# Kernel tuning notes

Measured on AMD Instinct MI355X. Metric: run time of the kernel, lower is better.

## Reference

```python
import jax, jax.numpy as jnp
import numpy as np

DIM_Q = 512
DIM_K = 512
DIM_V = 512
NUM_HEADS = 8
B, NQ, NK = 4, 2048, 2048


def _linear_init(key, d_in, d_out):
    kw, kb = jax.random.split(key)
    bound = 1.0 / np.sqrt(d_in)
    W = jax.random.uniform(kw, (d_in, d_out), minval=-bound, maxval=bound, dtype=jnp.float32)
    b = jax.random.uniform(kb, (d_out,), minval=-bound, maxval=bound, dtype=jnp.float32)
    return W, b


def setup_inputs() -> dict:
    key = jax.random.key(0)
    ks = jax.random.split(key, 6)
    Q = jax.random.normal(ks[0], (B, NQ, DIM_Q), dtype=jnp.float32)
    K = jax.random.normal(ks[1], (B, NK, DIM_K), dtype=jnp.float32)
    Wq, bq = _linear_init(ks[2], DIM_Q, DIM_V)
    Wk, bk = _linear_init(ks[3], DIM_K, DIM_V)
    Wv, bv = _linear_init(ks[4], DIM_K, DIM_V)
    Wo, bo = _linear_init(ks[5], DIM_V, DIM_V)
    ln0_g = jnp.ones((DIM_V,), jnp.float32)
    ln0_b = jnp.zeros((DIM_V,), jnp.float32)
    ln1_g = jnp.ones((DIM_V,), jnp.float32)
    ln1_b = jnp.zeros((DIM_V,), jnp.float32)
    return {"Q": Q, "K": K, "Wq": Wq, "bq": bq, "Wk": Wk, "bk": bk,
            "Wv": Wv, "bv": bv, "Wo": Wo, "bo": bo,
            "ln0_g": ln0_g, "ln0_b": ln0_b, "ln1_g": ln1_g, "ln1_b": ln1_b}


def _layer_norm(x, g, b, eps=1e-5):
    mu = jnp.mean(x, axis=-1, keepdims=True)
    var = jnp.mean(jnp.square(x - mu), axis=-1, keepdims=True)
    return (x - mu) * jax.lax.rsqrt(var + eps) * g + b


def reference(Q, K, Wq, bq, Wk, bk, Wv, bv, Wo, bo, ln0_g, ln0_b, ln1_g, ln1_b):
    h = NUM_HEADS
    dh = DIM_V // h
    q = Q @ Wq + bq                      # [B, NQ, DIM_V]
    k = K @ Wk + bk                      # [B, NK, DIM_V]
    v = K @ Wv + bv                      # [B, NK, DIM_V]
    qh = q.reshape(B, NQ, h, dh)
    kh = k.reshape(B, NK, h, dh)
    vh = v.reshape(B, NK, h, dh)
    # NOTE: faithful to original — scale by sqrt(dim_V), not sqrt(head_dim)
    scores = jnp.einsum('bqhd,bkhd->bhqk', qh, kh) / jnp.sqrt(jnp.float32(DIM_V))
    A = jax.nn.softmax(scores, axis=-1)  # [B, h, NQ, NK]
    o = jnp.einsum('bhqk,bkhd->bqhd', A, vh) + qh
    H = o.reshape(B, NQ, DIM_V)          # residual with projected Q
    H = _layer_norm(H, ln0_g, ln0_b)
    H = H + jax.nn.relu(H @ Wo + bo)
    H = _layer_norm(H, ln1_g, ln1_b)
    return H
```

## Files before the change

kernel.cpp:

```cpp
#include <hip/hip_runtime.h>

typedef float f32x4 __attribute__((ext_vector_type(4)));
typedef float f32x16 __attribute__((ext_vector_type(16)));
typedef __bf16 bf16x8 __attribute__((ext_vector_type(8)));
typedef unsigned short u16;
typedef unsigned int u32;
typedef u16 u16x8 __attribute__((ext_vector_type(8)));
typedef u16 u16x4 __attribute__((ext_vector_type(4)));
typedef u32 u32x4 __attribute__((ext_vector_type(4)));

#define SCALE2F (0.044194173824159216f * 1.4426950408889634f)
#define UNSCALE (1.0f / SCALE2F)

__device__ __forceinline__ u16 f2bf(float x){ return __builtin_bit_cast(u16, (__bf16)x); }
__device__ __forceinline__ float bf2f(u16 h){ unsigned u = ((unsigned)h) << 16; return __builtin_bit_cast(float, u); }
__device__ __forceinline__ int swz(int r, int byteInRow){ return (r*128 + byteInRow) ^ ((r & 7) << 4); }
__device__ __forceinline__ void gload16(const void* g, void* l) {
  __builtin_amdgcn_global_load_lds(
      (const __attribute__((address_space(1))) void*)g,
      (__attribute__((address_space(3))) void*)l, 16, 0, 0);
}
__device__ __forceinline__ u32 cvtpk(float lo, float hi_) {
  u32 r;
  asm("v_cvt_pk_bf16_f32 %0, %1, %2" : "=v"(r) : "v"(lo), "v"(hi_));
  return r;
}
__device__ __forceinline__ void swap32(u32 &a, u32 &b) {
  asm("v_permlane32_swap_b32 %0, %1" : "+v"(a), "+v"(b));
}

#define MFMA(a,b,c)   __builtin_amdgcn_mfma_f32_16x16x32_bf16((a),(b),(c),0,0,0)
#define MFMA32(a,b,c) __builtin_amdgcn_mfma_f32_32x32x16_bf16((a),(b),(c),0,0,0)

__global__ __launch_bounds__(256) void wprep_k(
    const float* __restrict__ W0, const float* __restrict__ W1,
    const float* __restrict__ W2, const float* __restrict__ W3,
    u16* __restrict__ wt)
{
  __shared__ float tile[64][68];
  const float* Ws[4] = {W0, W1, W2, W3};
  const float* W = Ws[blockIdx.z];
  const float sc = (blockIdx.z == 0) ? SCALE2F : 1.0f;
  u16* out = wt + (size_t)blockIdx.z * 512 * 512;
  int k0 = blockIdx.x * 64, n0 = blockIdx.y * 64;
  int t = threadIdx.x;
  #pragma unroll
  for (int i = 0; i < 2; ++i) {
    int c = t + i*256; int r = c >> 3, k8 = c & 7;
    const float* src = W + (size_t)(k0 + r)*512 + n0 + k8*8;
    *(f32x4*)&tile[r][k8*8]     = *(const f32x4*)src;
    *(f32x4*)&tile[r][k8*8 + 4] = *(const f32x4*)(src + 4);
  }
  __syncthreads();
  #pragma unroll
  for (int i = 0; i < 2; ++i) {
    int c = t + i*256; int r = c >> 3, k8 = c & 7;
    u16x8 h;
    #pragma unroll
    for (int j = 0; j < 8; ++j) h[j] = f2bf(tile[k8*8 + j][r] * sc);
    *(u16x8*)(out + (size_t)(n0 + r)*512 + k0 + k8*8) = h;
  }
}

__global__ __launch_bounds__(512) void proj2_k(
    const float* __restrict__ Qin, const float* __restrict__ Kin,
    const u16* __restrict__ wt,
    const float* __restrict__ bq, const float* __restrict__ bk, const float* __restrict__ bv,
    u16* __restrict__ qbuf, u16* __restrict__ kbuf, u16* __restrict__ vt)
{
  __shared__ __align__(16) u16 lA[2][64*64];
  __shared__ __align__(16) u16 lB0[2][128*64];
  __shared__ __align__(16) u16 lB1[2][128*64];
  int z = blockIdx.z;
  const float* A     = z ? Kin : Qin;
  const u16*   Bt0   = wt + (size_t)(z ? 1 : 0) * 262144;
  const u16*   Bt1   = wt + (size_t)2 * 262144;
  const float* bias0 = z ? bk : bq;
  const float bscale = z ? 1.0f : SCALE2F;
  int row0 = blockIdx.x * 64, col0 = blockIdx.y * 128;
  int t = threadIdx.x, lane = t & 63, wid = t >> 6;
  int wr = wid >> 2, wc = wid & 3;
  int l15 = lane & 15, lg = lane >> 4;
  int ar = t >> 3, ak8 = t & 7;
  int br = t >> 3;
  int bsrc = (((t & 7) << 4) ^ ((br & 7) << 4)) >> 1;
  const float* Arow = A + (size_t)row0 * 512;
  const u16*   B0row = Bt0 + (size_t)col0 * 512;
  const u16*   B1row = Bt1 + (size_t)col0 * 512;

  f32x4 acc0[2][2] = {}, acc1[2][2] = {};

  #pragma unroll
  for (int i = 0; i < 2; ++i)
    gload16(B0row + (size_t)(br + i*64)*512 + bsrc, (char*)lB0[0] + i*8192 + t*16);
  if (z) {
    #pragma unroll
    for (int i = 0; i < 2; ++i)
      gload16(B1row + (size_t)(br + i*64)*512 + bsrc, (char*)lB1[0] + i*8192 + t*16);
  }
  {
    const float* src = Arow + (size_t)ar*512 + ak8*8;
    f32x4 x0 = *(const f32x4*)src;
    f32x4 x1 = *(const f32x4*)(src + 4);
    u16x8 h;
    #pragma unroll
    for (int j = 0; j < 4; ++j) { h[j] = f2bf(x0[j]); h[j+4] = f2bf(x1[j]); }
    *(u16x8*)((char*)lA[0] + swz(ar, ak8*16)) = h;
  }
  __syncthreads();

  int cur = 0;
  for (int k0 = 0; k0 < 512; k0 += 64) {
    bool pf = (k0 + 64 < 512);
    f32x4 px0, px1;
    if (pf) {
      #pragma unroll
      for (int i = 0; i < 2; ++i)
        gload16(B0row + (size_t)(br + i*64)*512 + k0 + 64 + bsrc, (char*)lB0[cur^1] + i*8192 + t*16);
      if (z) {
        #pragma unroll
        for (int i = 0; i < 2; ++i)
          gload16(B1row + (size_t)(br + i*64)*512 + k0 + 64 + bsrc, (char*)lB1[cur^1] + i*8192 + t*16);
      }
      const float* src = Arow + (size_t)ar*512 + k0 + 64 + ak8*8;
      px0 = *(const f32x4*)src;
      px1 = *(const f32x4*)(src + 4);
    }
    const char* lAc = (const char*)lA[cur];
    const char* lB0c = (const char*)lB0[cur];
    const char* lB1c = (const char*)lB1[cur];
    #pragma unroll
    for (int ks = 0; ks < 2; ++ks) {
      bf16x8 af[2], b0f[2], b1f[2];
      #pragma unroll
      for (int m = 0; m < 2; ++m)
        af[m] = *(const bf16x8*)(lAc + swz(wr*32 + m*16 + l15, ks*64 + lg*16));
      #pragma unroll
      for (int n = 0; n < 2; ++n) {
        int rb = wc*32 + n*16 + l15;
        b0f[n] = *(const bf16x8*)(lB0c + swz(rb, ks*64 + lg*16));
        if (z) b1f[n] = *(const bf16x8*)(lB1c + swz(rb, ks*64 + lg*16));
      }
      #pragma unroll
      for (int m = 0; m < 2; ++m)
        #pragma unroll
        for (int n = 0; n < 2; ++n) {
          acc0[m][n] = MFMA(af[m], b0f[n], acc0[m][n]);
          if (z) acc1[m][n] = MFMA(af[m], b1f[n], acc1[m][n]);
        }
    }
    if (pf) {
      u16x8 h;
      #pragma unroll
      for (int j = 0; j < 4; ++j) { h[j] = f2bf(px0[j]); h[j+4] = f2bf(px1[j]); }
      *(u16x8*)((char*)lA[cur^1] + swz(ar, ak8*16)) = h;
    }
    __syncthreads();
    cur ^= 1;
  }

  u16* out0 = z ? kbuf : qbuf;
  #pragma unroll
  for (int m = 0; m < 2; ++m) {
    int rowg = row0 + wr*32 + m*16 + lg*4;
    #pragma unroll
    for (int n = 0; n < 2; ++n) {
      int colg = col0 + wc*32 + n*16 + l15;
      float bvv = bias0[colg] * bscale;
      #pragma unroll
      for (int r = 0; r < 4; ++r)
        out0[(size_t)(rowg + r)*512 + colg] = f2bf(acc0[m][n][r] + bvv);
    }
  }
  if (z) {
    #pragma unroll
    for (int m = 0; m < 2; ++m) {
      int rowg = row0 + wr*32 + m*16 + lg*4;
      int b = rowg >> 11, ntok = rowg & 2047;
      #pragma unroll
      for (int n = 0; n < 2; ++n) {
        int colg = col0 + wc*32 + n*16 + l15;
        float bvv = bv[colg];
        u16x4 hv;
        #pragma unroll
        for (int r = 0; r < 4; ++r) hv[r] = f2bf(acc1[m][n][r] + bvv);
        *(u16x4*)(vt + ((size_t)b*512 + colg)*2048 + ntok) = hv;
      }
    }
  }
}

__device__ __forceinline__ void mk_pb(const f32x16& s, float& ps, bf16x8& f0, bf16x8& f1) {
  float p[16];
  #pragma unroll
  for (int r = 0; r < 16; ++r) p[r] = __builtin_amdgcn_exp2f(s[r]);
  float t0 = (p[0] + p[1])  + (p[2] + p[3]);
  float t1 = (p[4] + p[5])  + (p[6] + p[7]);
  float t2 = (p[8] + p[9])  + (p[10] + p[11]);
  float t3 = (p[12] + p[13]) + (p[14] + p[15]);
  ps += (t0 + t1) + (t2 + t3);
  u32 a0 = cvtpk(p[0],  p[1]),  b0 = cvtpk(p[4],  p[5]);
  u32 a1 = cvtpk(p[2],  p[3]),  b1 = cvtpk(p[6],  p[7]);
  swap32(a0, b0); swap32(a1, b1);
  u32 a2 = cvtpk(p[8],  p[9]),  b2 = cvtpk(p[12], p[13]);
  u32 a3 = cvtpk(p[10], p[11]), b3 = cvtpk(p[14], p[15]);
  swap32(a2, b2); swap32(a3, b3);
  u32x4 w0 = {a0, a1, b0, b1};
  u32x4 w1 = {a2, a3, b2, b3};
  f0 = __builtin_bit_cast(bf16x8, w0);
  f1 = __builtin_bit_cast(bf16x8, w1);
}

__global__ __launch_bounds__(512, 4) void attn_k(
    const u16* __restrict__ qb, const u16* __restrict__ kb,
    const u16* __restrict__ vt, u16* __restrict__ ob)
{
  __shared__ __align__(16) char smem[65536];

  int t = threadIdx.x, lane = t & 63, wid = t >> 6;
  int bh = blockIdx.y, b = bh >> 3, h = bh & 7;
  int half = wid >> 2;
  int qw = wid & 3;
  int q0 = blockIdx.x * 128 + qw * 32;
  int l31 = lane & 31, hi = lane >> 5;

  const u16* kbase = kb + ((size_t)b*2048)*512 + h*64;
  const u16* vbase = vt + ((size_t)b*512 + h*64)*2048;

  int sr = t >> 3;
  int ssrc = ((t & 7) ^ (sr & 7)) << 3;

#define LKB(hf, bf) (smem + ((hf)*2 + (bf))*8192)
#define LVB(hf, bf) (smem + 32768 + ((hf)*2 + (bf))*8192)
#define STAGE(buf, off)                                                           \
  gload16(kbase + (size_t)((off) + sr)*512 + ssrc,        LKB(0,buf) + t*16);     \
  gload16(kbase + (size_t)((off) + 1024 + sr)*512 + ssrc, LKB(1,buf) + t*16);     \
  gload16(vbase + (size_t)sr*2048 + (off) + ssrc,         LVB(0,buf) + t*16);     \
  gload16(vbase + (size_t)sr*2048 + (off) + 1024 + ssrc,  LVB(1,buf) + t*16);

  bf16x8 aq[4];
  {
    const u16* qp = qb + ((size_t)(b*2048 + q0 + l31))*512 + h*64 + hi*8;
    #pragma unroll
    for (int ks = 0; ks < 4; ++ks) aq[ks] = *(const bf16x8*)(qp + ks*16);
  }

  f32x16 acc[2] = {};
  float ps = 0.0f;

  STAGE(0, 0);
  __syncthreads();

  int cur = 0;
  for (int i = 0; i < 16; ++i) {
    if (i + 1 < 16) { STAGE(cur^1, (i+1)*64); }
    const char* lKc = LKB(half, cur);
    const char* lVc = LVB(half, cur);
    bf16x8 pb[4];
    #pragma unroll
    for (int n = 0; n < 2; ++n) {
      f32x16 s = {};
      #pragma unroll
      for (int ks = 0; ks < 4; ++ks) {
        bf16x8 kf = *(const bf16x8*)(lKc + swz(n*32 + l31, ks*32 + hi*16));
        s = MFMA32(kf, aq[ks], s);
      }
      mk_pb(s, ps, pb[2*n], pb[2*n+1]);
    }
    #pragma unroll
    for (int m = 0; m < 2; ++m)
      #pragma unroll
      for (int ks = 0; ks < 4; ++ks) {
        bf16x8 vf = *(const bf16x8*)(lVc + swz(m*32 + l31, ks*32 + hi*16));
        acc[m] = MFMA32(vf, pb[ks], acc[m]);
      }
    __syncthreads();
    cur ^= 1;
  }
#undef STAGE

  ps += __shfl_xor(ps, 32, 64);
  float* cb = (float*)smem;
  if (half == 1) {
    float* dst = cb + qw * 2208;
    #pragma unroll
    for (int m = 0; m < 2; ++m)
      #pragma unroll
      for (int rq = 0; rq < 4; ++rq) {
        f32x4 v = {acc[m][rq*4], acc[m][rq*4+1], acc[m][rq*4+2], acc[m][rq*4+3]};
        *(f32x4*)(dst + l31*68 + m*32 + rq*8 + hi*4) = v;
      }
    if (hi == 0) dst[2176 + l31] = ps;
  }
  __syncthreads();
  if (half == 0) {
    const float* src = cb + qw * 2208;
    float inv = 1.0f / (ps + src[2176 + l31]);
    u16* obase = ob + ((size_t)(b*2048 + q0 + l31))*512 + h*64;
    const u16* qrb = qb + ((size_t)(b*2048 + q0 + l31))*512 + h*64;
    #pragma unroll
    for (int m = 0; m < 2; ++m)
      #pragma unroll
      for (int rq = 0; rq < 4; ++rq) {
        f32x4 other = *(const f32x4*)(src + l31*68 + m*32 + rq*8 + hi*4);
        u16x4 qr4 = *(const u16x4*)(qrb + m*32 + rq*8 + hi*4);
        u16x4 o4;
        #pragma unroll
        for (int e = 0; e < 4; ++e)
          o4[e] = f2bf((acc[m][rq*4 + e] + other[e])*inv + bf2f(qr4[e])*UNSCALE);
        *(u16x4*)(obase + m*32 + rq*8 + hi*4) = o4;
      }
  }
}

__global__ __launch_bounds__(512) void tail_k(
    const u16* __restrict__ ob, const u16* __restrict__ Bt,
    const float* __restrict__ bo,
    const float* __restrict__ g0, const float* __restrict__ b0,
    const float* __restrict__ g1, const float* __restrict__ b1,
    float* __restrict__ out)
{
  __shared__ __align__(16) u16 lA[2][32*64];
  __shared__ __align__(16) u16 lB[2][512*64];
  __shared__ float mu0[32], rs0[32], mu1[32], rs1[32];
  __shared__ float ps1[32][8], ss1[32][8];

  int row0 = blockIdx.x * 32;
  int t = threadIdx.x, lane = t & 63, wid = t >> 6;
  int l15 = lane & 15, lg = lane >> 4;

  {
    int r = t >> 4, c0 = (t & 15) * 32;
    const u16* xp = ob + (size_t)(row0 + r)*512 + c0;
    float s = 0.0f, ss = 0.0f;
    #pragma unroll
    for (int j = 0; j < 4; ++j) {
      u16x8 v = *(const u16x8*)(xp + j*8);
      #pragma unroll
      for (int e = 0; e < 8; ++e) { float f = bf2f(v[e]); s += f; ss += f*f; }
    }
    #pragma unroll
    for (int m = 1; m < 16; m <<= 1) { s += __shfl_xor(s, m, 64); ss += __shfl_xor(ss, m, 64); }
    if ((t & 15) == 0) {
      float mu = s * (1.0f/512.0f);
      float var = ss * (1.0f/512.0f) - mu*mu;
      mu0[r] = mu; rs0[r] = rsqrtf(var + 1e-5f);
    }
  }
  __syncthreads();

  int ar = t >> 3, ak8 = t & 7;
  int br = t >> 3;
  int bsrc = ((t & 7) ^ (br & 7)) << 3;

  auto stageA = [&](int buf, int k0) {
    if (t < 256) {
      u16x8 x = *(const u16x8*)(ob + (size_t)(row0 + ar)*512 + k0 + ak8*8);
      f32x4 gv0 = *(const f32x4*)(g0 + k0 + ak8*8);
      f32x4 gv1 = *(const f32x4*)(g0 + k0 + ak8*8 + 4);
      f32x4 bv0 = *(const f32x4*)(b0 + k0 + ak8*8);
      f32x4 bv1 = *(const f32x4*)(b0 + k0 + ak8*8 + 4);
      float mu = mu0[ar], rs = rs0[ar];
      u16x8 h;
      #pragma unroll
      for (int j = 0; j < 4; ++j) {
        h[j]   = f2bf((bf2f(x[j])   - mu)*rs*gv0[j] + bv0[j]);
        h[j+4] = f2bf((bf2f(x[j+4]) - mu)*rs*gv1[j] + bv1[j]);
      }
      *(u16x8*)((char*)lA[buf] + swz(ar, ak8*16)) = h;
    }
  };

  #pragma unroll
  for (int i = 0; i < 8; ++i)
    gload16(Bt + (size_t)(br + i*64)*512 + bsrc, (char*)lB[0] + i*8192 + t*16);
  stageA(0, 0);
  __syncthreads();

  f32x4 acc[2][4] = {};
  int cur = 0;
  for (int k0 = 0; k0 < 512; k0 += 64) {
    if (k0 + 64 < 512) {
      #pragma unroll
      for (int i = 0; i < 8; ++i)
        gload16(Bt + (size_t)(br + i*64)*512 + k0 + 64 + bsrc, (char*)lB[cur^1] + i*8192 + t*16);
      stageA(cur^1, k0 + 64);
    }
    const char* lAc = (const char*)lA[cur];
    const char* lBc = (const char*)lB[cur];
    #pragma unroll
    for (int ks = 0; ks < 2; ++ks) {
      bf16x8 af[2], bfv[4];
      #pragma unroll
      for (int m = 0; m < 2; ++m)
        af[m] = *(const bf16x8*)(lAc + swz(m*16 + l15, ks*64 + lg*16));
      #pragma unroll
      for (int n = 0; n < 4; ++n)
        bfv[n] = *(const bf16x8*)(lBc + swz(wid*64 + n*16 + l15, ks*64 + lg*16));
      #pragma unroll
      for (int m = 0; m < 2; ++m)
        #pragma unroll
        for (int n = 0; n < 4; ++n)
          acc[m][n] = MFMA(af[m], bfv[n], acc[m][n]);
    }
    __syncthreads();
    cur ^= 1;
  }

  float Gv[2][4][4];
  float sp[2][4] = {}, ssp[2][4] = {};
  #pragma unroll
  for (int n = 0; n < 4; ++n) {
    int colg = wid*64 + n*16 + l15;
    float bov = bo[colg];
    float g0c = g0[colg], b0c = b0[colg];
    #pragma unroll
    for (int m = 0; m < 2; ++m) {
      #pragma unroll
      for (int rr = 0; rr < 4; ++rr) {
        int rit = m*16 + lg*4 + rr;
        float H = (bf2f(ob[(size_t)(row0 + rit)*512 + colg]) - mu0[rit])*rs0[rit]*g0c + b0c;
        float G = H + fmaxf(acc[m][n][rr] + bov, 0.0f);
        Gv[m][n][rr] = G;
        sp[m][rr] += G;
        ssp[m][rr] += G*G;
      }
    }
  }
  #pragma unroll
  for (int msk = 1; msk < 16; msk <<= 1)
    #pragma unroll
    for (int m = 0; m < 2; ++m)
      #pragma unroll
      for (int rr = 0; rr < 4; ++rr) {
        sp[m][rr]  += __shfl_xor(sp[m][rr],  msk, 64);
        ssp[m][rr] += __shfl_xor(ssp[m][rr], msk, 64);
      }
  if (l15 == 0) {
    #pragma unroll
    for (int m = 0; m < 2; ++m)
      #pragma unroll
      for (int rr = 0; rr < 4; ++rr) {
        int rit = m*16 + lg*4 + rr;
        ps1[rit][wid] = sp[m][rr];
        ss1[rit][wid] = ssp[m][rr];
      }
  }
  __syncthreads();
  if (t < 32) {
    float s = 0.0f, ss = 0.0f;
    #pragma unroll
    for (int w = 0; w < 8; ++w) { s += ps1[t][w]; ss += ss1[t][w]; }
    float mu = s * (1.0f/512.0f);
    float var = ss * (1.0f/512.0f) - mu*mu;
    mu1[t] = mu; rs1[t] = rsqrtf(var + 1e-5f);
  }
  __syncthreads();
  #pragma unroll
  for (int n = 0; n < 4; ++n) {
    int colg = wid*64 + n*16 + l15;
    float g1c = g1[colg], b1c = b1[colg];
    #pragma unroll
    for (int m = 0; m < 2; ++m)
      #pragma unroll
      for (int rr = 0; rr < 4; ++rr) {
        int rit = m*16 + lg*4 + rr;
        out[(size_t)(row0 + rit)*512 + colg] =
            (Gv[m][n][rr] - mu1[rit])*rs1[rit]*g1c + b1c;
      }
  }
}

extern "C" void kernel_launch(void* const* d_in, const int* in_sizes, int n_in,
                              void* d_out, int out_size, void* d_ws, size_t ws_size,
                              hipStream_t stream)
{
  const float* Q   = (const float*)d_in[0];
  const float* K   = (const float*)d_in[1];
  const float* Wq  = (const float*)d_in[2];
  const float* bq  = (const float*)d_in[3];
  const float* Wk  = (const float*)d_in[4];
  const float* bk  = (const float*)d_in[5];
  const float* Wv  = (const float*)d_in[6];
  const float* bv  = (const float*)d_in[7];
  const float* Wo  = (const float*)d_in[8];
  const float* bo  = (const float*)d_in[9];
  const float* g0  = (const float*)d_in[10];
  const float* b0  = (const float*)d_in[11];
  const float* g1  = (const float*)d_in[12];
  const float* b1  = (const float*)d_in[13];

  char* ws = (char*)d_ws;
  u16*   wt    = (u16*)(ws + 0);
  u16*   qbuf  = (u16*)(ws + (2u<<20));
  u16*   kbuf  = (u16*)(ws + (10u<<20));
  u16*   vt    = (u16*)(ws + (18u<<20));
  u16*   ob    = (u16*)(ws + (26u<<20));

  wprep_k<<<dim3(8, 8, 4), 256, 0, stream>>>(Wq, Wk, Wv, Wo, wt);
  proj2_k<<<dim3(128, 4, 2), 512, 0, stream>>>(Q, K, wt, bq, bk, bv, qbuf, kbuf, vt);
  attn_k<<<dim3(16, 32), 512, 0, stream>>>(qbuf, kbuf, vt, ob);
  tail_k<<<256, 512, 0, stream>>>(ob, wt + 3*262144, bo, g0, b0, g1, b1, (float*)d_out);
}
```

Baseline: 95.60 us.

## Split QKV projection into uniform 128x128 tiles and remap attention blocks per XCD

The projection kernel no longer fuses K and V GEMMs in one block with an imbalanced z split. It now runs three uniform GEMMs as 768 blocks with 128x128 tiles, which gives every block the same work and more reuse per A tile. The cost is converting K from fp32 to bf16 twice, once for the K GEMM and once for the V GEMM. Separately, the attention grid is flattened and remapped so that all query tiles of one (batch, head) land on the same XCD, aiming to improve L2 reuse of K/V.

New measurement: 107.2 us. 1.12x slower.

```diff
diff --git a/kernel.cpp b/kernel.cpp
--- a/kernel.cpp
+++ b/kernel.cpp
@@ -62,128 +62,112 @@
   }
 }
 
-__global__ __launch_bounds__(512) void proj2_k(
+__global__ __launch_bounds__(512) void proj_k(
     const float* __restrict__ Qin, const float* __restrict__ Kin,
     const u16* __restrict__ wt,
     const float* __restrict__ bq, const float* __restrict__ bk, const float* __restrict__ bv,
     u16* __restrict__ qbuf, u16* __restrict__ kbuf, u16* __restrict__ vt)
 {
-  __shared__ __align__(16) u16 lA[2][64*64];
-  __shared__ __align__(16) u16 lB0[2][128*64];
-  __shared__ __align__(16) u16 lB1[2][128*64];
-  int z = blockIdx.z;
-  const float* A     = z ? Kin : Qin;
-  const u16*   Bt0   = wt + (size_t)(z ? 1 : 0) * 262144;
-  const u16*   Bt1   = wt + (size_t)2 * 262144;
-  const float* bias0 = z ? bk : bq;
-  const float bscale = z ? 1.0f : SCALE2F;
-  int row0 = blockIdx.x * 64, col0 = blockIdx.y * 128;
+  __shared__ __align__(16) u16 lA[2][128*64];
+  __shared__ __align__(16) u16 lB[2][128*64];
+  int gid = blockIdx.x;
+  int gemm = gid >> 8;
+  int rem = gid & 255;
+  int row0 = (rem >> 2) * 128;
+  int col0 = (rem & 3) * 128;
+  const float* A    = (gemm == 0) ? Qin : Kin;
+  const u16*   Bt   = wt + (size_t)gemm * 262144;
+  const float* bias = (gemm == 0) ? bq : (gemm == 1) ? bk : bv;
+  const float bscale = (gemm == 0) ? SCALE2F : 1.0f;
+
   int t = threadIdx.x, lane = t & 63, wid = t >> 6;
   int wr = wid >> 2, wc = wid & 3;
   int l15 = lane & 15, lg = lane >> 4;
-  int ar = t >> 3, ak8 = t & 7;
+  int at = t >> 2, aq = t & 3;
   int br = t >> 3;
-  int bsrc = (((t & 7) << 4) ^ ((br & 7) << 4)) >> 1;
+  int bsrc = ((t & 7) ^ (br & 7)) << 3;
   const float* Arow = A + (size_t)row0 * 512;
-  const u16*   B0row = Bt0 + (size_t)col0 * 512;
-  const u16*   B1row = Bt1 + (size_t)col0 * 512;
-
-  f32x4 acc0[2][2] = {}, acc1[2][2] = {};
-
-  #pragma unroll
-  for (int i = 0; i < 2; ++i)
-    gload16(B0row + (size_t)(br + i*64)*512 + bsrc, (char*)lB0[0] + i*8192 + t*16);
-  if (z) {
-    #pragma unroll
-    for (int i = 0; i < 2; ++i)
-      gload16(B1row + (size_t)(br + i*64)*512 + bsrc, (char*)lB1[0] + i*8192 + t*16);
-  }
-  {
-    const float* src = Arow + (size_t)ar*512 + ak8*8;
+  const u16*   Brow = Bt + (size_t)col0 * 512;
+
+  f32x4 acc[4][2] = {};
+
+  auto stageA = [&](int buf, int k0) {
+    const float* src = Arow + (size_t)at*512 + k0 + aq*16;
     f32x4 x0 = *(const f32x4*)src;
     f32x4 x1 = *(const f32x4*)(src + 4);
-    u16x8 h;
-    #pragma unroll
-    for (int j = 0; j < 4; ++j) { h[j] = f2bf(x0[j]); h[j+4] = f2bf(x1[j]); }
-    *(u16x8*)((char*)lA[0] + swz(ar, ak8*16)) = h;
-  }
+    f32x4 x2 = *(const f32x4*)(src + 8);
+    f32x4 x3 = *(const f32x4*)(src + 12);
+    u16x8 h0, h1;
+    #pragma unroll
+    for (int j = 0; j < 4; ++j) {
+      h0[j] = f2bf(x0[j]); h0[j+4] = f2bf(x1[j]);
+      h1[j] = f2bf(x2[j]); h1[j+4] = f2bf(x3[j]);
+    }
+    *(u16x8*)((char*)lA[buf] + swz(at, aq*32))      = h0;
+    *(u16x8*)((char*)lA[buf] + swz(at, aq*32 + 16)) = h1;
+  };
+
+  #pragma unroll
+  for (int i = 0; i < 2; ++i)
+    gload16(Brow + (size_t)(br + i*64)*512 + bsrc, (char*)lB[0] + i*8192 + t*16);
+  stageA(0, 0);
   __syncthreads();
 
   int cur = 0;
   for (int k0 = 0; k0 < 512; k0 += 64) {
-    bool pf = (k0 + 64 < 512);
-    f32x4 px0, px1;
-    if (pf) {
+    if (k0 + 64 < 512) {
       #pragma unroll
       for (int i = 0; i < 2; ++i)
-        gload16(B0row + (size_t)(br + i*64)*512 + k0 + 64 + bsrc, (char*)lB0[cur^1] + i*8192 + t*16);
-      if (z) {
+        gload16(Brow + (size_t)(br + i*64)*512 + k0 + 64 + bsrc, (char*)lB[cur^1] + i*8192 + t*16);
+      stageA(cur^1, k0 + 64);
+    }
+    const char* lAc = (const char*)lA[cur];
+    const char* lBc = (const char*)lB[cur];
+    #pragma unroll
+    for (int ks = 0; ks < 2; ++ks) {
+      bf16x8 af[4], bf[2];
+      #pragma unroll
+      for (int m = 0; m < 4; ++m)
+        af[m] = *(const bf16x8*)(lAc + swz(wr*64 + m*16 + l15, ks*64 + lg*16));
+      #pragma unroll
+      for (int n = 0; n < 2; ++n)
+        bf[n] = *(const bf16x8*)(lBc + swz(wc*32 + n*16 + l15, ks*64 + lg*16));
+      #pragma unroll
+      for (int m = 0; m < 4; ++m)
         #pragma unroll
-        for (int i = 0; i < 2; ++i)
-          gload16(B1row + (size_t)(br + i*64)*512 + k0 + 64 + bsrc, (char*)lB1[cur^1] + i*8192 + t*16);
-      }
-      const float* src = Arow + (size_t)ar*512 + k0 + 64 + ak8*8;
-      px0 = *(const f32x4*)src;
-      px1 = *(const f32x4*)(src + 4);
-    }
-    const char* lAc = (const char*)lA[cur];
-    const char* lB0c = (const char*)lB0[cur];
-    const char* lB1c = (const char*)lB1[cur];
-    #pragma unroll
-    for (int ks = 0; ks < 2; ++ks) {
-      bf16x8 af[2], b0f[2], b1f[2];
-      #pragma unroll
-      for (int m = 0; m < 2; ++m)
-        af[m] = *(const bf16x8*)(lAc + swz(wr*32 + m*16 + l15, ks*64 + lg*16));
-      #pragma unroll
-      for (int n = 0; n < 2; ++n) {
-        int rb = wc*32 + n*16 + l15;
-        b0f[n] = *(const bf16x8*)(lB0c + swz(rb, ks*64 + lg*16));
-        if (z) b1f[n] = *(const bf16x8*)(lB1c + swz(rb, ks*64 + lg*16));
-      }
-      #pragma unroll
-      for (int m = 0; m < 2; ++m)
-        #pragma unroll
-        for (int n = 0; n < 2; ++n) {
-          acc0[m][n] = MFMA(af[m], b0f[n], acc0[m][n]);
-          if (z) acc1[m][n] = MFMA(af[m], b1f[n], acc1[m][n]);
-        }
-    }
-    if (pf) {
-      u16x8 h;
-      #pragma unroll
-      for (int j = 0; j < 4; ++j) { h[j] = f2bf(px0[j]); h[j+4] = f2bf(px1[j]); }
-      *(u16x8*)((char*)lA[cur^1] + swz(ar, ak8*16)) = h;
+        for (int n = 0; n < 2; ++n)
+          acc[m][n] = MFMA(af[m], bf[n], acc[m][n]);
     }
     __syncthreads();
     cur ^= 1;
   }
 
-  u16* out0 = z ? kbuf : qbuf;
-  #pragma unroll
-  for (int m = 0; m < 2; ++m) {
-    int rowg = row0 + wr*32 + m*16 + lg*4;
-    #pragma unroll
-    for (int n = 0; n < 2; ++n) {
-      int colg = col0 + wc*32 + n*16 + l15;
-      float bvv = bias0[colg] * bscale;
-      #pragma unroll
-      for (int r = 0; r < 4; ++r)
-        out0[(size_t)(rowg + r)*512 + colg] = f2bf(acc0[m][n][r] + bvv);
-    }
-  }
-  if (z) {
-    #pragma unroll
-    for (int m = 0; m < 2; ++m) {
-      int rowg = row0 + wr*32 + m*16 + lg*4;
-      int b = rowg >> 11, ntok = rowg & 2047;
+  if (gemm < 2) {
+    u16* out = gemm ? kbuf : qbuf;
+    #pragma unroll
+    for (int m = 0; m < 4; ++m) {
+      int rowg = row0 + wr*64 + m*16 + lg*4;
       #pragma unroll
       for (int n = 0; n < 2; ++n) {
         int colg = col0 + wc*32 + n*16 + l15;
-        float bvv = bv[colg];
+        float bvv = bias[colg] * bscale;
+        #pragma unroll
+        for (int r = 0; r < 4; ++r)
+          out[(size_t)(rowg + r)*512 + colg] = f2bf(acc[m][n][r] + bvv);
+      }
+    }
+  } else {
+    #pragma unroll
+    for (int m = 0; m < 4; ++m) {
+      int rowg = row0 + wr*64 + m*16 + lg*4;
+      int b = rowg >> 11, ntok = rowg & 2047;
+      #pragma unroll
+      for (int n = 0; n < 2; ++n) {
+        int colg = col0 + wc*32 + n*16 + l15;
+        float bvv = bias[colg];
         u16x4 hv;
         #pragma unroll
-        for (int r = 0; r < 4; ++r) hv[r] = f2bf(acc1[m][n][r] + bvv);
+        for (int r = 0; r < 4; ++r) hv[r] = f2bf(acc[m][n][r] + bvv);
         *(u16x4*)(vt + ((size_t)b*512 + colg)*2048 + ntok) = hv;
       }
     }
@@ -218,10 +202,14 @@
   __shared__ __align__(16) char smem[65536];
 
   int t = threadIdx.x, lane = t & 63, wid = t >> 6;
-  int bh = blockIdx.y, b = bh >> 3, h = bh & 7;
+  int j = blockIdx.x;
+  int xcd = j & 7, slot = j >> 3;
+  int qx = slot & 15;
+  int bh = ((slot >> 4) << 3) | xcd;
+  int b = bh >> 3, h = bh & 7;
   int half = wid >> 2;
   int qw = wid & 3;
-  int q0 = blockIdx.x * 128 + qw * 32;
+  int q0 = qx * 128 + qw * 32;
   int l31 = lane & 31, hi = lane >> 5;
 
   const u16* kbase = kb + ((size_t)b*2048)*512 + h*64;
@@ -498,7 +486,7 @@
   u16*   ob    = (u16*)(ws + (26u<<20));
 
   wprep_k<<<dim3(8, 8, 4), 256, 0, stream>>>(Wq, Wk, Wv, Wo, wt);
-  proj2_k<<<dim3(128, 4, 2), 512, 0, stream>>>(Q, K, wt, bq, bk, bv, qbuf, kbuf, vt);
-  attn_k<<<dim3(16, 32), 512, 0, stream>>>(qbuf, kbuf, vt, ob);
+  proj_k<<<768, 512, 0, stream>>>(Q, K, wt, bq, bk, bv, qbuf, kbuf, vt);
+  attn_k<<<512, 512, 0, stream>>>(qbuf, kbuf, vt, ob);
   tail_k<<<256, 512, 0, stream>>>(ob, wt + 3*262144, bo, g0, b0, g1, b1, (float*)d_out);
 }
```

## Pre-convert Q/K to bf16 and remap attention blocks across XCDs

Applied to the files above, without the earlier changes.

Adds a separate conversion kernel that turns the fp32 Q and K inputs into bf16 buffers. The projection kernel can then stage its A tiles with async global-to-LDS loads like the weights, instead of loading through registers and converting in the loop. The attention grid becomes 1D with a block-index remap so that blocks sharing a batch-head land on the same XCD, aiming for better L2 reuse of K/V. The cost is an extra kernel launch and an extra pass that writes and rereads Q/K in bf16.

Result: slower. 98.93 us (+3.5%).

```diff
diff --git a/kernel.cpp b/kernel.cpp
--- a/kernel.cpp
+++ b/kernel.cpp
@@ -62,8 +62,23 @@
   }
 }
 
+__global__ __launch_bounds__(256) void conv_k(
+    const float* __restrict__ s0, const float* __restrict__ s1,
+    u16* __restrict__ d0, u16* __restrict__ d1)
+{
+  const float* s = blockIdx.y ? s1 : s0;
+  u16* d = blockIdx.y ? d1 : d0;
+  size_t i = ((size_t)blockIdx.x * 256 + threadIdx.x) * 8;
+  f32x4 a = *(const f32x4*)(s + i);
+  f32x4 b = *(const f32x4*)(s + i + 4);
+  u16x8 h;
+  #pragma unroll
+  for (int j = 0; j < 4; ++j) { h[j] = f2bf(a[j]); h[j+4] = f2bf(b[j]); }
+  *(u16x8*)(d + i) = h;
+}
+
 __global__ __launch_bounds__(512) void proj2_k(
-    const float* __restrict__ Qin, const float* __restrict__ Kin,
+    const u16* __restrict__ Qbf, const u16* __restrict__ Kbf,
     const u16* __restrict__ wt,
     const float* __restrict__ bq, const float* __restrict__ bk, const float* __restrict__ bv,
     u16* __restrict__ qbuf, u16* __restrict__ kbuf, u16* __restrict__ vt)
@@ -72,7 +87,7 @@
   __shared__ __align__(16) u16 lB0[2][128*64];
   __shared__ __align__(16) u16 lB1[2][128*64];
   int z = blockIdx.z;
-  const float* A     = z ? Kin : Qin;
+  const u16*   A     = z ? Kbf : Qbf;
   const u16*   Bt0   = wt + (size_t)(z ? 1 : 0) * 262144;
   const u16*   Bt1   = wt + (size_t)2 * 262144;
   const float* bias0 = z ? bk : bq;
@@ -81,51 +96,29 @@
   int t = threadIdx.x, lane = t & 63, wid = t >> 6;
   int wr = wid >> 2, wc = wid & 3;
   int l15 = lane & 15, lg = lane >> 4;
-  int ar = t >> 3, ak8 = t & 7;
-  int br = t >> 3;
-  int bsrc = (((t & 7) << 4) ^ ((br & 7) << 4)) >> 1;
-  const float* Arow = A + (size_t)row0 * 512;
-  const u16*   B0row = Bt0 + (size_t)col0 * 512;
-  const u16*   B1row = Bt1 + (size_t)col0 * 512;
+  int ar = t >> 3;
+  int asrc = ((t & 7) ^ (ar & 7)) << 3;
+  const u16* Arow  = A + (size_t)row0 * 512;
+  const u16* B0row = Bt0 + (size_t)col0 * 512;
+  const u16* B1row = Bt1 + (size_t)col0 * 512;
 
   f32x4 acc0[2][2] = {}, acc1[2][2] = {};
 
-  #pragma unroll
-  for (int i = 0; i < 2; ++i)
-    gload16(B0row + (size_t)(br + i*64)*512 + bsrc, (char*)lB0[0] + i*8192 + t*16);
-  if (z) {
-    #pragma unroll
-    for (int i = 0; i < 2; ++i)
-      gload16(B1row + (size_t)(br + i*64)*512 + bsrc, (char*)lB1[0] + i*8192 + t*16);
-  }
-  {
-    const float* src = Arow + (size_t)ar*512 + ak8*8;
-    f32x4 x0 = *(const f32x4*)src;
-    f32x4 x1 = *(const f32x4*)(src + 4);
-    u16x8 h;
-    #pragma unroll
-    for (int j = 0; j < 4; ++j) { h[j] = f2bf(x0[j]); h[j+4] = f2bf(x1[j]); }
-    *(u16x8*)((char*)lA[0] + swz(ar, ak8*16)) = h;
-  }
+#define STG(buf, k0)                                                                         \
+  gload16(Arow + (size_t)ar*512 + (k0) + asrc, (char*)lA[buf] + t*16);                       \
+  gload16(B0row + (size_t)ar*512 + (k0) + asrc, (char*)lB0[buf] + t*16);                     \
+  gload16(B0row + (size_t)(ar + 64)*512 + (k0) + asrc, (char*)lB0[buf] + 8192 + t*16);       \
+  if (z) {                                                                                   \
+    gload16(B1row + (size_t)ar*512 + (k0) + asrc, (char*)lB1[buf] + t*16);                   \
+    gload16(B1row + (size_t)(ar + 64)*512 + (k0) + asrc, (char*)lB1[buf] + 8192 + t*16);     \
+  }
+
+  STG(0, 0);
   __syncthreads();
 
   int cur = 0;
   for (int k0 = 0; k0 < 512; k0 += 64) {
-    bool pf = (k0 + 64 < 512);
-    f32x4 px0, px1;
-    if (pf) {
-      #pragma unroll
-      for (int i = 0; i < 2; ++i)
-        gload16(B0row + (size_t)(br + i*64)*512 + k0 + 64 + bsrc, (char*)lB0[cur^1] + i*8192 + t*16);
-      if (z) {
-        #pragma unroll
-        for (int i = 0; i < 2; ++i)
-          gload16(B1row + (size_t)(br + i*64)*512 + k0 + 64 + bsrc, (char*)lB1[cur^1] + i*8192 + t*16);
-      }
-      const float* src = Arow + (size_t)ar*512 + k0 + 64 + ak8*8;
-      px0 = *(const f32x4*)src;
-      px1 = *(const f32x4*)(src + 4);
-    }
+    if (k0 + 64 < 512) { STG(cur^1, k0 + 64); }
     const char* lAc = (const char*)lA[cur];
     const char* lB0c = (const char*)lB0[cur];
     const char* lB1c = (const char*)lB1[cur];
@@ -149,15 +142,10 @@
           if (z) acc1[m][n] = MFMA(af[m], b1f[n], acc1[m][n]);
         }
     }
-    if (pf) {
-      u16x8 h;
-      #pragma unroll
-      for (int j = 0; j < 4; ++j) { h[j] = f2bf(px0[j]); h[j+4] = f2bf(px1[j]); }
-      *(u16x8*)((char*)lA[cur^1] + swz(ar, ak8*16)) = h;
-    }
     __syncthreads();
     cur ^= 1;
   }
+#undef STG
 
   u16* out0 = z ? kbuf : qbuf;
   #pragma unroll
@@ -218,10 +206,14 @@
   __shared__ __align__(16) char smem[65536];
 
   int t = threadIdx.x, lane = t & 63, wid = t >> 6;
-  int bh = blockIdx.y, b = bh >> 3, h = bh & 7;
+  int j = blockIdx.x;
+  int xcd = j & 7, slot = j >> 3;
+  int qx = slot & 15;
+  int bh = ((slot >> 4) << 3) | xcd;
+  int b = bh >> 3, h = bh & 7;
   int half = wid >> 2;
   int qw = wid & 3;
-  int q0 = blockIdx.x * 128 + qw * 32;
+  int q0 = qx * 128 + qw * 32;
   int l31 = lane & 31, hi = lane >> 5;
 
   const u16* kbase = kb + ((size_t)b*2048)*512 + h*64;
@@ -496,9 +488,12 @@
   u16*   kbuf  = (u16*)(ws + (10u<<20));
   u16*   vt    = (u16*)(ws + (18u<<20));
   u16*   ob    = (u16*)(ws + (26u<<20));
+  u16*   Qbf   = (u16*)(ws + (34u<<20));
+  u16*   Kbf   = (u16*)(ws + (43u<<20));
 
   wprep_k<<<dim3(8, 8, 4), 256, 0, stream>>>(Wq, Wk, Wv, Wo, wt);
-  proj2_k<<<dim3(128, 4, 2), 512, 0, stream>>>(Q, K, wt, bq, bk, bv, qbuf, kbuf, vt);
-  attn_k<<<dim3(16, 32), 512, 0, stream>>>(qbuf, kbuf, vt, ob);
+  conv_k<<<dim3(2048, 2), 256, 0, stream>>>(Q, K, Qbf, Kbf);
+  proj2_k<<<dim3(128, 4, 2), 512, 0, stream>>>(Qbf, Kbf, wt, bq, bk, bv, qbuf, kbuf, vt);
+  attn_k<<<512, 512, 0, stream>>>(qbuf, kbuf, vt, ob);
   tail_k<<<256, 512, 0, stream>>>(ob, wt + 3*262144, bo, g0, b0, g1, b1, (float*)d_out);
 }
```
